# Optimization experiments

Measured on AMD Instinct MI355X. Metric: run time of the kernel, lower is better.

Reference implementation:

```python
import jax, jax.numpy as jnp
import numpy as np

V, B, NT, EN, EMB, ODIM = 5000, 512, 50, 200, 200, 40
PERP = 30.0
BETA_TEMP = 0.2
SINKHORN_ALPHA = 20.0
WEIGHT_ECR = 250.0
ECR_ITERS = 100
SNE_ITERS = 20
EPS_DIV = 1e-16


def _pairwise_sq(x, y):
    # ||x_i||^2 + ||y_j||^2 - 2 x_i . y_j  (matches module's pairwise_euclidean_distance)
    return (jnp.sum(x * x, axis=1)[:, None] + jnp.sum(y * y, axis=1)[None, :]
            - 2.0 * (x @ y.T))


def _bn_train(x, g, b):
    # BatchNorm1d, training mode: batch statistics, biased variance
    m = x.mean(axis=0)
    v = x.var(axis=0)
    return (x - m) / jnp.sqrt(v + 1e-5) * g + b


def _snekhorn_reduce(X, proj):
    # SNEkhorn-style symmetric entropic affinity on rows of X (log-domain
    # symmetric Sinkhorn with uniform marginals), followed by a linear readout
    # to ODIM dims. X: (n, d) -> (n, ODIM).
    C = _pairwise_sq(X, X)                       # (n, n)
    n = X.shape[0]
    eps = jnp.mean(C) / jnp.log(PERP) + 1e-6     # bandwidth tied to perplexity
    log_a = -jnp.log(float(n))                   # uniform target marginal

    @jax.checkpoint
    def step(f, _):
        lse = jax.nn.logsumexp((f[None, :] - C) / eps, axis=1)
        f = 0.5 * (f + eps * (log_a - lse))      # symmetric Sinkhorn update
        return f, None

    f, _ = jax.lax.scan(step, jnp.zeros(n, C.dtype), None, length=SNE_ITERS)
    P = jnp.exp((f[:, None] + f[None, :] - C) / eps)  # (n, n) affinity
    return P @ proj                                   # (n, ODIM)


def _ecr_loss(cost):
    # ECR: entropic OT between topic and word embeddings (fixed-iteration Sinkhorn)
    Km = jnp.exp(-cost * SINKHORN_ALPHA)          # (NT, V)
    a = jnp.full((NT, 1), 1.0 / NT, cost.dtype)
    bm = jnp.full((V, 1), 1.0 / V, cost.dtype)

    def step(u, _):
        v = bm / (Km.T @ u + EPS_DIV)
        u = a / (Km @ v + EPS_DIV)
        return u, None

    u, _ = jax.lax.scan(step, jnp.full((NT, 1), 1.0 / NT, cost.dtype), None,
                        length=ECR_ITERS)
    v = bm / (Km.T @ u + EPS_DIV)
    transp = u * (Km * v.T)
    return WEIGHT_ECR * jnp.sum(transp * cost)


def setup_inputs() -> dict:
    key = jax.random.key(0)
    ks = jax.random.split(key, 12)

    def nrm(k, shape, s=0.02):
        return jax.random.normal(k, shape, jnp.float32) * s

    word_emb = jax.random.normal(ks[0], (V, EMB), jnp.float32)
    word_emb = word_emb / jnp.linalg.norm(word_emb, axis=1, keepdims=True)
    topic_emb = jax.random.normal(ks[1], (NT, EMB), jnp.float32) * 0.1
    topic_emb = topic_emb / jnp.linalg.norm(topic_emb, axis=1, keepdims=True)

    return dict(
        bow=jax.random.uniform(ks[2], (B, V), jnp.float32),
        eps_noise=jax.random.normal(ks[3], (ODIM, NT), jnp.float32),
        W1=nrm(ks[4], (EN, V)), b1=jnp.zeros(EN, jnp.float32),
        W2=nrm(ks[5], (EN, EN)), b2=jnp.zeros(EN, jnp.float32),
        Wmu=nrm(ks[6], (NT, EN)), bmu=jnp.zeros(NT, jnp.float32),
        Wlv=nrm(ks[7], (NT, EN)), blv=jnp.zeros(NT, jnp.float32),
        g_mu=jnp.ones(NT, jnp.float32), be_mu=jnp.zeros(NT, jnp.float32),
        g_lv=jnp.ones(NT, jnp.float32), be_lv=jnp.zeros(NT, jnp.float32),
        g_dec=jnp.ones(V, jnp.float32), be_dec=jnp.zeros(V, jnp.float32),
        word_emb=word_emb, topic_emb=topic_emb,
        proj_V=nrm(ks[8], (V, ODIM), 1.0),
        proj_K=nrm(ks[9], (NT, ODIM), 1.0),
    )


def reference(bow, eps_noise, W1, b1, W2, b2, Wmu, bmu, Wlv, blv,
              g_mu, be_mu, g_lv, be_lv, g_dec, be_dec,
              word_emb, topic_emb, proj_V, proj_K):
    # bow_reduced = SNEkhorn(bow.T).T : (ODIM, V)
    bow_reduced = _snekhorn_reduce(bow.T, proj_V).T

    # encoder1: Linear -> softplus -> Linear -> softplus
    e1 = jax.nn.softplus(bow_reduced @ W1.T + b1)
    e1 = jax.nn.softplus(e1 @ W2.T + b2)
    mu = _bn_train(e1 @ Wmu.T + bmu, g_mu, be_mu)        # (ODIM, NT)
    logvar = _bn_train(e1 @ Wlv.T + blv, g_lv, be_lv)

    z = mu + eps_noise * jnp.exp(0.5 * logvar)           # reparameterize (training)
    theta = jax.nn.softmax(z, axis=1)                    # (ODIM, NT)
    theta_reduced = _snekhorn_reduce(theta.T, proj_K).T  # (ODIM, NT)

    # KL vs logistic-normal prior; with a = ones: mu2 = 0, var2 = 1 - 1/NT
    var2 = 1.0 - 1.0 / NT
    var = jnp.exp(logvar)
    kld = 0.5 * ((var / var2 + mu * mu / var2 + jnp.log(var2) - logvar).sum(axis=1) - NT)
    loss_KL = kld.mean()

    # beta + decode (cost computed once; torch code computes it twice identically)
    cost = _pairwise_sq(topic_emb, word_emb)             # (NT, V)
    beta = jax.nn.softmax(-cost / BETA_TEMP, axis=0)
    recon = jax.nn.softmax(_bn_train(theta_reduced @ beta, g_dec, be_dec), axis=-1)
    recon_loss = -(bow_reduced * jnp.log(recon)).sum(axis=1).mean()

    loss_TM = recon_loss + loss_KL
    loss_ECR = _ecr_loss(cost)
    loss = loss_TM + loss_ECR
    return loss, loss_TM, loss_ECR, theta_reduced
```

## Files before the change

kernel.cpp:

```cpp
#include <hip/hip_runtime.h>
#include <hip/hip_bf16.h>
#include <hip/hip_fp16.h>

#define VV 5000
#define NTOP 50
#define ENH 200
#define NEMB 200
#define OD 40
#define MP 5120
#define KNS 5008

typedef __attribute__((ext_vector_type(8))) short short8;
typedef __attribute__((ext_vector_type(4))) float f32x4;

constexpr size_t OFF_R      = 0;
constexpr size_t OFF_S      = 20224;
constexpr size_t OFF_SCAL   = 22528;
constexpr size_t OFF_PHIA   = 22784;
constexpr size_t OFF_PHIB   = 43008;
constexpr size_t OFF_ROWS   = 63232;
constexpr size_t OFF_PARTS  = 63744;
constexpr size_t OFF_FLAGS  = 71936;
constexpr size_t OFF_MUPRE  = 72960;
constexpr size_t OFF_LVPRE  = 81152;
constexpr size_t OFF_E1T    = 89344;
constexpr size_t OFF_E2T    = 121600;
constexpr size_t OFF_THRED  = 153856;
constexpr size_t OFF_BOWRED = 162048;
constexpr size_t ZERO_BYTES = 962304;
constexpr size_t OFF_PVT    = 962304;
constexpr size_t OFF_XB     = 1453824;
constexpr size_t OFF_CE     = 6696704;
constexpr size_t OFF_COST   = 56696832;
constexpr size_t OFF_KM     = 57697024;
constexpr size_t OFF_BETA   = 58697216;
constexpr size_t OFF_RN     = 59697408;

__device__ __forceinline__ void ecr_block(int b, int it_base, int n_iters, bool do_final,
    const __half* __restrict__ Kn, const float* __restrict__ cost,
    float* __restrict__ acc, int* __restrict__ cnt, float* __restrict__ scal,
    char* smem){
  __half* KmL = (__half*)smem;
  float* varr = (float*)(smem + 32208);
  float* us   = (float*)(smem + 33488);
  float* p5   = (float*)(smem + 33696);
  float* redr = (float*)(smem + 34736);
  const int t = threadIdx.x;
  const int base = (b < 8) ? b*313 : 2504 + (b-8)*312;
  const int sz   = (b < 8) ? 313 : 312;
  for (int c = t; c < 322; c += 256){
    if (c < sz){
      #pragma unroll
      for (int q = 0; q < NTOP; ++q)
        KmL[q*322 + c] = Kn[(size_t)q*KNS + base + c];
    } else {
      #pragma unroll
      for (int q = 0; q < NTOP; ++q) KmL[q*322 + c] = __float2half(0.f);
    }
  }
  if (t < 52){
    float u0 = 0.f;
    if (t < NTOP){
      if (it_base == 0) u0 = 1.f/(float)NTOP;
      else {
        float sm = __hip_atomic_load(&acc[((it_base-1)%3)*64 + t],
                                     __ATOMIC_RELAXED, __HIP_MEMORY_SCOPE_AGENT);
        u0 = (1.f/(float)NTOP)/(sm + 1e-16f);
      }
    }
    us[t] = u0;
  }
  for (int c = sz + t; c < 320; c += 256) varr[c] = 0.f;
  __syncthreads();
  const bool act = (2*t < sz);
  for (int k = 0; k < n_iters; ++k){
    const int g = it_base + k;
    if (act){
      float w0 = 0.f, w1 = 0.f, w2 = 0.f, w3 = 0.f;
      #pragma unroll
      for (int q = 0; q < NTOP; q += 2){
        float u0 = us[q], u1 = us[q+1];
        float2 f0 = __half22float2(*(const __half2*)(KmL + q*322 + 2*t));
        float2 f1 = __half22float2(*(const __half2*)(KmL + (q+1)*322 + 2*t));
        w0 += f0.x*u0; w1 += f0.y*u0;
        w2 += f1.x*u1; w3 += f1.y*u1;
      }
      float2 vv;
      vv.x = (1.f/(float)VV)/((w0+w2) + 1e-16f);
      vv.y = (2*t+1 < sz) ? (1.f/(float)VV)/((w1+w3) + 1e-16f) : 0.f;
      *(float2*)(varr + 2*t) = vv;
    }
    __syncthreads();
    if (t < 250){
      const int qq = t % NTOP, stripe = t / NTOP;
      const __half* kp = KmL + qq*322 + stripe*64;
      const float* vp = varr + stripe*64;
      float s0 = 0.f, s1 = 0.f, s2 = 0.f, s3 = 0.f;
      #pragma unroll
      for (int n = 0; n < 64; n += 4){
        float2 fa = __half22float2(*(const __half2*)(kp + n));
        float2 fb = __half22float2(*(const __half2*)(kp + n + 2));
        float4 v4 = *(const float4*)(vp + n);
        s0 += fa.x*v4.x; s1 += fa.y*v4.y; s2 += fb.x*v4.z; s3 += fb.y*v4.w;
      }
      p5[stripe*52 + qq] = (s0+s1)+(s2+s3);
    }
    __syncthreads();
    if (t < NTOP){
      float sm = p5[t] + p5[52+t] + p5[104+t] + p5[156+t] + p5[208+t];
      __hip_atomic_fetch_add(&acc[(g%3)*64 + t], sm,
                             __ATOMIC_RELAXED, __HIP_MEMORY_SCOPE_AGENT);
    }
    __asm__ volatile("s_waitcnt vmcnt(0)" ::: "memory");
    if (t == 0){
      __hip_atomic_fetch_add(cnt, 1, __ATOMIC_RELEASE, __HIP_MEMORY_SCOPE_AGENT);
      const int tgt = 16*(g+1);
      while (__hip_atomic_load(cnt, __ATOMIC_ACQUIRE, __HIP_MEMORY_SCOPE_AGENT) < tgt)
        __builtin_amdgcn_s_sleep(1);
    }
    if (t < NTOP){
      float sm = __hip_atomic_load(&acc[(g%3)*64 + t],
                                   __ATOMIC_RELAXED, __HIP_MEMORY_SCOPE_AGENT);
      us[t] = (1.f/(float)NTOP)/(sm + 1e-16f);
    }
    if (t < 64)
      __hip_atomic_store(&acc[((g+2)%3)*64 + t], 0.f,
                         __ATOMIC_RELAXED, __HIP_MEMORY_SCOPE_AGENT);
    __syncthreads();
  }
  if (!do_final) return;
  float lsum = 0.f;
  if (act){
    float w0 = 0.f, w1 = 0.f, w2 = 0.f, w3 = 0.f;
    #pragma unroll
    for (int q = 0; q < NTOP; q += 2){
      float u0 = us[q], u1 = us[q+1];
      float2 f0 = __half22float2(*(const __half2*)(KmL + q*322 + 2*t));
      float2 f1 = __half22float2(*(const __half2*)(KmL + (q+1)*322 + 2*t));
      w0 += f0.x*u0; w1 += f0.y*u0;
      w2 += f1.x*u1; w3 += f1.y*u1;
    }
    float v0 = (1.f/(float)VV)/((w0+w2) + 1e-16f);
    const bool ok1 = (2*t+1 < sz);
    float v1 = ok1 ? (1.f/(float)VV)/((w1+w3) + 1e-16f) : 0.f;
    float accv = 0.f;
    #pragma unroll
    for (int q = 0; q < NTOP; ++q){
      float2 f = __half22float2(*(const __half2*)(KmL + q*322 + 2*t));
      float uq = us[q];
      float c0 = cost[(size_t)q*VV + base + 2*t];
      accv += uq*f.x*v0*c0;
      if (ok1){
        float c1 = cost[(size_t)q*VV + base + 2*t + 1];
        accv += uq*f.y*v1*c1;
      }
    }
    lsum = accv;
  }
  #pragma unroll
  for (int off = 32; off; off >>= 1) lsum += __shfl_down(lsum, off, 64);
  if ((t & 63) == 0) redr[t >> 6] = lsum;
  __syncthreads();
  if (t == 0) atomicAdd(&scal[3], redr[0]+redr[1]+redr[2]+redr[3]);
}

__global__ __launch_bounds__(256) void k1_stats(const float* __restrict__ bow,
    __hip_bfloat16* __restrict__ Xb, float* __restrict__ r, float* __restrict__ s,
    const __half* __restrict__ Kn, const float* __restrict__ cost,
    float* __restrict__ accg, int* __restrict__ cnt, float* __restrict__ scal){
  __shared__ __align__(16) char smem[34816];
  const int t = threadIdx.x;
  if (blockIdx.x >= 40){
    int b = (blockIdx.x - 40)*8 + blockIdx.y;
    ecr_block(b, 0, 15, false, Kn, cost, accg, cnt, scal, smem);
    return;
  }
  float (*lds)[129] = (float(*)[129])smem;
  const int i0 = blockIdx.x * 128, d0 = blockIdx.y * 64;
  #pragma unroll
  for (int m = 0; m < 32; ++m){
    int idx = m*256 + t;
    int di = idx >> 7;
    int ii = idx & 127;
    int gi = i0 + ii;
    lds[di][ii] = (gi < VV) ? bow[(size_t)(d0+di)*VV + gi] : 0.f;
  }
  __syncthreads();
  if (t < 128 && (i0 + t) < VV){
    float acc = 0.f;
    for (int di = 0; di < 64; ++di){ float v = lds[di][t]; acc += v*v; }
    atomicAdd(&r[i0+t], acc);
  }
  if (t < 64){
    float acc = 0.f;
    for (int ii = 0; ii < 128; ++ii) acc += lds[t][ii];
    atomicAdd(&s[d0+t], acc);
  }
  __syncthreads();
  #pragma unroll
  for (int m = 0; m < 32; ++m){
    int idx = m*256 + t;
    int ii = idx >> 6;
    int dd = idx & 63;
    Xb[(size_t)(i0+ii)*512 + d0 + dd] = __float2bfloat16(lds[dd][ii]);
  }
}

__global__ __launch_bounds__(256) void k2_eps(const float* __restrict__ r,
    const float* __restrict__ s, float* __restrict__ scal){
  const int t = threadIdx.x;
  float a = 0.f, b = 0.f;
  for (int i = t; i < VV; i += 256) a += r[i];
  for (int d = t; d < 512; d += 256){ float v = s[d]; b += v*v; }
  #pragma unroll
  for (int off = 32; off; off >>= 1){
    a += __shfl_down(a, off, 64);
    b += __shfl_down(b, off, 64);
  }
  __shared__ float ra[4], rb[4];
  int lane = t & 63, w = t >> 6;
  if (lane == 0){ ra[w] = a; rb[w] = b; }
  __syncthreads();
  if (t == 0){
    float sa = ra[0]+ra[1]+ra[2]+ra[3];
    float sb = rb[0]+rb[1]+rb[2]+rb[3];
    float meanC = 2.f*sa/(float)VV - 2.f*sb/((float)VV*(float)VV);
    float eps = meanC / logf(30.f) + 1e-6f;
    scal[0] = eps;
    scal[1] = 1.f/eps;
  }
}

__global__ __launch_bounds__(256) void k3_gemm_ecr(const __hip_bfloat16* __restrict__ Xb,
    const float* __restrict__ r, float* __restrict__ scal, __half* __restrict__ Ce,
    const __half* __restrict__ Kn, const float* __restrict__ cost,
    float* __restrict__ accg, int* __restrict__ cnt){
  __shared__ __align__(16) char smem[36864];
  if (blockIdx.x < 16){
    ecr_block(blockIdx.x, 15, 25, false, Kn, cost, accg, cnt, scal, smem);
    return;
  }
  __hip_bfloat16* As = (__hip_bfloat16*)smem;
  __hip_bfloat16* Bs = (__hip_bfloat16*)(smem + 128*72*2);
  const int b2 = blockIdx.x - 16;
  const int t = threadIdx.x;
  const int i0 = (b2 % 40) * 128, j0 = (b2 / 40) * 128;
  const int lane = t & 63, w = t >> 6;
  const int wr = w >> 1, wc = w & 1;
  const int m16 = lane & 15, q4 = lane >> 4;
  f32x4 acc[4][4];
  #pragma unroll
  for (int a = 0; a < 4; ++a)
    #pragma unroll
    for (int b = 0; b < 4; ++b) acc[a][b] = (f32x4){0.f,0.f,0.f,0.f};
  const int srow = t >> 3, sseg = t & 7;
  for (int kc = 0; kc < 512; kc += 64){
    __syncthreads();
    #pragma unroll
    for (int m = 0; m < 4; ++m){
      int row = m*32 + srow;
      uint4 va = *(const uint4*)(Xb + (size_t)(i0+row)*512 + kc + sseg*8);
      *(uint4*)(As + row*72 + sseg*8) = va;
      uint4 vb = *(const uint4*)(Xb + (size_t)(j0+row)*512 + kc + sseg*8);
      *(uint4*)(Bs + row*72 + sseg*8) = vb;
    }
    __syncthreads();
    #pragma unroll
    for (int ks = 0; ks < 64; ks += 32){
      short8 af[4], bf[4];
      #pragma unroll
      for (int f = 0; f < 4; ++f){
        af[f] = *(const short8*)(As + (wr*64 + f*16 + m16)*72 + ks + q4*8);
        bf[f] = *(const short8*)(Bs + (wc*64 + f*16 + m16)*72 + ks + q4*8);
      }
      #pragma unroll
      for (int fr = 0; fr < 4; ++fr)
        #pragma unroll
        for (int fc = 0; fc < 4; ++fc)
          acc[fr][fc] = __builtin_amdgcn_mfma_f32_16x16x32_bf16(af[fr], bf[fc], acc[fr][fc], 0, 0, 0);
    }
  }
  const float inv_eps = scal[1];
  #pragma unroll
  for (int fr = 0; fr < 4; ++fr){
    int rbase = i0 + wr*64 + fr*16 + q4*4;
    #pragma unroll
    for (int fc = 0; fc < 4; ++fc){
      int col = j0 + wc*64 + fc*16 + m16;
      if (col < VV){
        float rc = r[col];
        #pragma unroll
        for (int q = 0; q < 4; ++q){
          int row = rbase + q;
          if (row < VV){
            float val = (r[row] + rc - 2.f*acc[fr][fc][q]) * inv_eps;
            Ce[(size_t)row*VV + col] = __float2half(val);
          }
        }
      }
    }
  }
}

__global__ __launch_bounds__(256) void k4_sweep_ecr(const __half* __restrict__ Ce,
    const float* __restrict__ phi_prev, float* __restrict__ phi_cur,
    const float* __restrict__ ssum_prev, float* __restrict__ ssum_next,
    float* __restrict__ ssum_zero,
    const __half* __restrict__ Kn, const float* __restrict__ cost,
    float* __restrict__ accg, int* __restrict__ cnt, float* __restrict__ scal,
    int it_base, int g){
  __shared__ __align__(16) char smem[34816];
  const int t = threadIdx.x;
  if (blockIdx.x < 16){
    ecr_block(blockIdx.x, it_base, 2, false, Kn, cost, accg, cnt, scal, smem);
    return;
  }
  const int sb = blockIdx.x - 16;
  const int i0 = (sb >> 1) * 8;
  const int h  = sb & 1;
  const int u0 = h ? 312 : 0;
  const int u1 = h ? 625 : 312;
  const int jbase = u0 * 8;
  const int ncol = (u1 - u0) * 8;
  float* pj  = (float*)smem;
  float* red = (float*)smem + 2504;
  const float loga = -8.517193191416238f;
  for (int j = t; j < ncol; j += 256){
    int gj = jbase + j;
    pj[j] = (g == 0) ? 0.f
          : 0.5f*(phi_prev[gj] + loga - __logf(ssum_prev[gj]));
  }
  if (g > 0 && sb < 20 && t < 250){
    int i = sb*250 + t;
    phi_cur[i] = 0.5f*(phi_prev[i] + loga - __logf(ssum_prev[i]));
  }
  if (sb >= 20 && sb < 40 && t < 250)
    ssum_zero[(sb-20)*250 + t] = 0.f;
  __syncthreads();
  float acc[8];
  #pragma unroll
  for (int rr = 0; rr < 8; ++rr) acc[rr] = 0.f;
  const uint4* ce0 = (const uint4*)(Ce + (size_t)i0*VV);
  for (int u = u0 + t; u < u1; u += 256){
    int lj = (u - u0)*8;
    float p[8];
    #pragma unroll
    for (int e = 0; e < 8; ++e) p[e] = pj[lj + e];
    #pragma unroll
    for (int rr = 0; rr < 8; ++rr){
      uint4 v = ce0[(size_t)rr*625 + u];
      const __half2* hp = (const __half2*)&v;
      float2 c0 = __half22float2(hp[0]);
      float2 c1 = __half22float2(hp[1]);
      float2 c2 = __half22float2(hp[2]);
      float2 c3 = __half22float2(hp[3]);
      acc[rr] += __expf(p[0] - c0.x) + __expf(p[1] - c0.y)
               + __expf(p[2] - c1.x) + __expf(p[3] - c1.y)
               + __expf(p[4] - c2.x) + __expf(p[5] - c2.y)
               + __expf(p[6] - c3.x) + __expf(p[7] - c3.y);
    }
  }
  #pragma unroll
  for (int rr = 0; rr < 8; ++rr)
    #pragma unroll
    for (int off = 32; off; off >>= 1)
      acc[rr] += __shfl_down(acc[rr], off, 64);
  int lane = t & 63, w = t >> 6;
  if (lane == 0){
    #pragma unroll
    for (int rr = 0; rr < 8; ++rr) red[w*8 + rr] = acc[rr];
  }
  __syncthreads();
  if (t < 8){
    float psum = red[t] + red[8+t] + red[16+t] + red[24+t];
    atomicAdd(&ssum_next[i0 + t], psum);
  }
}

__global__ __launch_bounds__(256) void k5p_pvt(const float* __restrict__ projV,
    __hip_bfloat16* __restrict__ pvt, const float* __restrict__ phi19,
    const float* __restrict__ ssum19, float* __restrict__ phiF){
  const int t = threadIdx.x;
  if (blockIdx.x < 20){
    if (t < 250){
      int i = blockIdx.x*250 + t;
      phiF[i] = 0.5f*(phi19[i] + (-8.517193191416238f) - __logf(ssum19[i]));
    }
    return;
  }
  int idx = (blockIdx.x - 20)*256 + t;
  if (idx >= 48*MP) return;
  int n = idx / MP, j = idx - n*MP;
  float v = (n < OD && j < VV) ? projV[(size_t)j*OD + n] : 0.f;
  pvt[idx] = __float2bfloat16(v);
}

__global__ __launch_bounds__(256) void k5_bowred(const __half* __restrict__ Ce,
    const float* __restrict__ phi, const __hip_bfloat16* __restrict__ pvt,
    float* __restrict__ brpA, float* __restrict__ brpC, float* __restrict__ brpD,
    const __half* __restrict__ Kn, const float* __restrict__ cost,
    float* __restrict__ accg, int* __restrict__ cnt, float* __restrict__ scal){
  __shared__ __align__(16) char smem[34816];
  const int t = threadIdx.x;
  if (blockIdx.x >= 40){
    int b = (blockIdx.x - 40)*8 + blockIdx.y;
    ecr_block(b, 80, 15, false, Kn, cost, accg, cnt, scal, smem);
    return;
  }
  __hip_bfloat16* As = (__hip_bfloat16*)smem;
  __hip_bfloat16* Bs = (__hip_bfloat16*)(smem + 18432);
  const int i0 = blockIdx.x * 128;
  const int k0 = blockIdx.y * 640;
  const int lane = t & 63, w = t >> 6;
  const int m16 = lane & 15, q4 = lane >> 4;
  f32x4 acc[2][3];
  #pragma unroll
  for (int a = 0; a < 2; ++a)
    #pragma unroll
    for (int b = 0; b < 3; ++b) acc[a][b] = (f32x4){0.f,0.f,0.f,0.f};
  for (int kc = k0; kc < k0 + 640; kc += 64){
    __syncthreads();
    #pragma unroll
    for (int m = 0; m < 4; ++m){
      int g = m*256 + t;
      int row = g >> 3, cg = g & 7;
      int gi = i0 + row, j2 = kc + cg*8;
      union { __hip_bfloat16 h[8]; short8 v; } u;
      if (gi < VV && j2 < VV){
        uint4 vce = *(const uint4*)(Ce + (size_t)gi*VV + j2);
        const __half2* hp = (const __half2*)&vce;
        float pb = phi[gi];
        float4 pj0 = *(const float4*)(phi + j2);
        float4 pj1 = *(const float4*)(phi + j2 + 4);
        float pj[8] = {pj0.x,pj0.y,pj0.z,pj0.w,pj1.x,pj1.y,pj1.z,pj1.w};
        #pragma unroll
        for (int e = 0; e < 4; ++e){
          float2 ce = __half22float2(hp[e]);
          u.h[2*e]   = __float2bfloat16(__expf(pb + pj[2*e]   - ce.x));
          u.h[2*e+1] = __float2bfloat16(__expf(pb + pj[2*e+1] - ce.y));
        }
      } else {
        #pragma unroll
        for (int e = 0; e < 8; ++e) u.h[e] = __float2bfloat16(0.f);
      }
      *(short8*)(As + row*72 + cg*8) = u.v;
    }
    #pragma unroll
    for (int m = 0; m < 12; ++m){
      int idx = m*256 + t;
      int row = idx >> 6, c = idx & 63;
      Bs[row*72 + c] = pvt[(size_t)row*MP + kc + c];
    }
    __syncthreads();
    #pragma unroll
    for (int ks = 0; ks < 64; ks += 32){
      short8 af[2], bf[3];
      #pragma unroll
      for (int f = 0; f < 2; ++f)
        af[f] = *(const short8*)(As + (w*32 + f*16 + m16)*72 + ks + q4*8);
      #pragma unroll
      for (int f = 0; f < 3; ++f)
        bf[f] = *(const short8*)(Bs + (f*16 + m16)*72 + ks + q4*8);
      #pragma unroll
      for (int fr = 0; fr < 2; ++fr)
        #pragma unroll
        for (int fc = 0; fc < 3; ++fc)
          acc[fr][fc] = __builtin_amdgcn_mfma_f32_16x16x32_bf16(af[fr], bf[fc], acc[fr][fc], 0, 0, 0);
    }
  }
  __syncthreads();
  float* LF = (float*)smem;
  #pragma unroll
  for (int fr = 0; fr < 2; ++fr){
    int lr = w*32 + fr*16 + q4*4;
    #pragma unroll
    for (int fc = 0; fc < 3; ++fc){
      int col = fc*16 + m16;
      #pragma unroll
      for (int q = 0; q < 4; ++q)
        LF[col*133 + lr + q] = acc[fr][fc][q];
    }
  }
  __syncthreads();
  float* brp = (blockIdx.y < 6) ? brpA + (size_t)blockIdx.y*200000
             : (blockIdx.y == 6) ? brpC : brpD;
  for (int o = t; o < OD*128; o += 256){
    int col = o >> 7, row = o & 127;
    int gr = i0 + row;
    if (gr < VV) brp[(size_t)col*VV + gr] = LF[col*133 + row];
  }
}

__global__ __launch_bounds__(256) void k5r_red(const float* __restrict__ brpA,
    const float* __restrict__ brpC, const float* __restrict__ brpD,
    float* __restrict__ br){
  int idx = blockIdx.x*256 + threadIdx.x;
  if (idx >= 50000) return;
  const float4* a = (const float4*)brpA;
  float4 s = a[idx];
  #pragma unroll
  for (int sl = 1; sl < 6; ++sl){
    float4 v = a[(size_t)sl*50000 + idx];
    s.x += v.x; s.y += v.y; s.z += v.z; s.w += v.w;
  }
  {
    float4 v = ((const float4*)brpC)[idx];
    s.x += v.x; s.y += v.y; s.z += v.z; s.w += v.w;
  }
  {
    float4 v = ((const float4*)brpD)[idx];
    s.x += v.x; s.y += v.y; s.z += v.z; s.w += v.w;
  }
  ((float4*)br)[idx] = s;
}

__global__ __launch_bounds__(256) void k6_e1(const float* __restrict__ br,
    const float* __restrict__ W1, float* __restrict__ e1pre,
    const __half* __restrict__ Kn, const float* __restrict__ cost,
    float* __restrict__ accg, int* __restrict__ cnt, float* __restrict__ scal){
  __shared__ __align__(16) char smem[34816];
  const int t = threadIdx.x;
  if (blockIdx.y == 10){
    if (blockIdx.x < 16)
      ecr_block(blockIdx.x, 95, 5, true, Kn, cost, accg, cnt, scal, smem);
    return;
  }
  const int lane = t & 63, w = t >> 6;
  const int k = blockIdx.x*4 + w;
  const int f0 = blockIdx.y * 125;
  float acc[OD];
  #pragma unroll
  for (int i = 0; i < OD; ++i) acc[i] = 0.f;
  const float4* w4p = (const float4*)(W1 + (size_t)k*VV);
  for (int f4 = f0 + lane; f4 < f0 + 125; f4 += 64){
    float4 wv = w4p[f4];
    #pragma unroll
    for (int i = 0; i < OD; ++i){
      float4 bv = ((const float4*)(br + (size_t)i*VV))[f4];
      acc[i] += bv.x*wv.x + bv.y*wv.y + bv.z*wv.z + bv.w*wv.w;
    }
  }
  #pragma unroll
  for (int i = 0; i < OD; ++i)
    #pragma unroll
    for (int off = 32; off; off >>= 1)
      acc[i] += __shfl_down(acc[i], off, 64);
  float (*red)[OD] = (float(*)[OD])smem;
  if (lane == 0){
    #pragma unroll
    for (int i = 0; i < OD; ++i) red[w][i] = acc[i];
  }
  __syncthreads();
  if (t < 160){
    int ww = t / OD, i = t - ww*OD;
    int kk = blockIdx.x*4 + ww;
    atomicAdd(&e1pre[kk*OD + i], red[ww][i]);
  }
}

__global__ __launch_bounds__(256) void k6b_sp(const float* __restrict__ b1,
    float* __restrict__ e1t){
  int idx = blockIdx.x*256 + threadIdx.x;
  if (idx >= ENH*OD) return;
  int kk = idx / OD;
  float x = e1t[idx] + b1[kk];
  e1t[idx] = (x > 20.f) ? x : log1pf(__expf(x));
}

__global__ __launch_bounds__(256) void k7_e2(const float* __restrict__ e1t,
    const float* __restrict__ W2, const float* __restrict__ b2, float* __restrict__ e2t){
  const int t = threadIdx.x;
  const int lane = t & 63, w = t >> 6;
  const int k = blockIdx.x*4 + w;
  float acc[OD];
  #pragma unroll
  for (int i = 0; i < OD; ++i) acc[i] = 0.f;
  for (int j = lane; j < ENH; j += 64){
    float wv = W2[(size_t)k*ENH + j];
    #pragma unroll
    for (int i = 0; i < OD; ++i) acc[i] += e1t[j*OD + i] * wv;
  }
  #pragma unroll
  for (int i = 0; i < OD; ++i)
    #pragma unroll
    for (int off = 32; off; off >>= 1)
      acc[i] += __shfl_down(acc[i], off, 64);
  __shared__ float red[4][OD];
  if (lane == 0){
    #pragma unroll
    for (int i = 0; i < OD; ++i) red[w][i] = acc[i];
  }
  __syncthreads();
  if (t < 160){
    int ww = t / OD, i = t - ww*OD;
    int kk = blockIdx.x*4 + ww;
    float x = red[ww][i] + b2[kk];
    float sp = (x > 20.f) ? x : log1pf(__expf(x));
    e2t[kk*OD + i] = sp;
  }
}

__global__ __launch_bounds__(256) void k8a_mulv(const float* __restrict__ e2t,
    const float* __restrict__ Wmu, const float* __restrict__ bmu,
    const float* __restrict__ Wlv, const float* __restrict__ blv,
    float* __restrict__ mupre, float* __restrict__ lvpre){
  int id = blockIdx.x*256 + threadIdx.x;
  if (id >= NTOP*OD) return;
  int t50 = id / OD, i = id - t50*OD;
  float am = 0.f, al = 0.f;
  for (int kk = 0; kk < ENH; ++kk){
    float e = e2t[kk*OD + i];
    am += e * Wmu[t50*ENH + kk];
    al += e * Wlv[t50*ENH + kk];
  }
  mupre[t50*OD + i] = am + bmu[t50];
  lvpre[t50*OD + i] = al + blv[t50];
}

__global__ __launch_bounds__(256) void k8b_theta(const float* __restrict__ mupre,
    const float* __restrict__ lvpre,
    const float* __restrict__ g_mu, const float* __restrict__ be_mu,
    const float* __restrict__ g_lv, const float* __restrict__ be_lv,
    const float* __restrict__ eps_noise, const float* __restrict__ projK,
    float* __restrict__ thred, float* __restrict__ d_out3, float* __restrict__ scal){
  __shared__ float mu[NTOP][OD];
  __shared__ float lv[NTOP][OD];
  __shared__ float th[OD][NTOP];
  __shared__ float C2[NTOP][NTOP];
  __shared__ float P2[NTOP][NTOP];
  __shared__ float f2[NTOP], nf[NTOP];
  __shared__ float sred[4];
  __shared__ float eps2s[2];
  const int t = threadIdx.x;
  if (t < NTOP){
    float m = 0.f;
    for (int i = 0; i < OD; ++i) m += mupre[t*OD + i];
    m *= (1.f/OD);
    float v = 0.f;
    for (int i = 0; i < OD; ++i){ float d = mupre[t*OD+i] - m; v += d*d; }
    v *= (1.f/OD);
    float sc = g_mu[t] * rsqrtf(v + 1e-5f);
    float sh = be_mu[t];
    for (int i = 0; i < OD; ++i) mu[t][i] = (mupre[t*OD+i] - m)*sc + sh;
    m = 0.f;
    for (int i = 0; i < OD; ++i) m += lvpre[t*OD + i];
    m *= (1.f/OD);
    v = 0.f;
    for (int i = 0; i < OD; ++i){ float d = lvpre[t*OD+i] - m; v += d*d; }
    v *= (1.f/OD);
    sc = g_lv[t] * rsqrtf(v + 1e-5f);
    sh = be_lv[t];
    for (int i = 0; i < OD; ++i) lv[t][i] = (lvpre[t*OD+i] - m)*sc + sh;
  }
  __syncthreads();
  {
    float kl = 0.f;
    if (t < OD){
      const float var2 = 1.f - 1.f/(float)NTOP;
      const float lv2 = logf(var2);
      float ssum = 0.f;
      for (int q = 0; q < NTOP; ++q){
        float l = lv[q][t];
        float m = mu[q][t];
        ssum += (__expf(l) + m*m)/var2 + lv2 - l;
      }
      kl = 0.5f*(ssum - (float)NTOP);
    }
    #pragma unroll
    for (int off = 32; off; off >>= 1) kl += __shfl_down(kl, off, 64);
    if ((t & 63) == 0) sred[t >> 6] = kl;
    __syncthreads();
    if (t == 0) scal[2] = (sred[0]+sred[1]+sred[2]+sred[3]) * (1.f/OD);
    __syncthreads();
  }
  if (t < OD){
    float z[NTOP];
    float mx = -1e30f;
    for (int q = 0; q < NTOP; ++q){
      float val = mu[q][t] + eps_noise[t*NTOP + q]*__expf(0.5f*lv[q][t]);
      z[q] = val;
      mx = fmaxf(mx, val);
    }
    float ssum = 0.f;
    for (int q = 0; q < NTOP; ++q){ float e = __expf(z[q]-mx); z[q] = e; ssum += e; }
    float inv = 1.f/ssum;
    for (int q = 0; q < NTOP; ++q) th[t][q] = z[q]*inv;
  }
  __syncthreads();
  {
    float csum = 0.f;
    for (int pr = t; pr < NTOP*NTOP; pr += 256){
      int a = pr / NTOP, b = pr - (pr/NTOP)*NTOP;
      float ss = 0.f;
      for (int i = 0; i < OD; ++i){ float d = th[i][a] - th[i][b]; ss += d*d; }
      C2[a][b] = ss;
      csum += ss;
    }
    #pragma unroll
    for (int off = 32; off; off >>= 1) csum += __shfl_down(csum, off, 64);
    if ((t & 63) == 0) sred[t >> 6] = csum;
    __syncthreads();
    if (t == 0){
      float meanC = (sred[0]+sred[1]+sred[2]+sred[3]) / ((float)NTOP*NTOP);
      float e2 = meanC / logf(30.f) + 1e-6f;
      eps2s[0] = e2; eps2s[1] = 1.f/e2;
    }
  }
  if (t < NTOP) f2[t] = 0.f;
  __syncthreads();
  const float loga2 = -logf((float)NTOP);
  for (int it = 0; it < 20; ++it){
    if (t < NTOP){
      float ie = eps2s[1];
      float ssum = 0.f;
      for (int sI = 0; sI < NTOP; ++sI)
        ssum += __expf((f2[sI] - C2[t][sI]) * ie);
      float lse = __logf(ssum);
      nf[t] = 0.5f*(f2[t] + eps2s[0]*(loga2 - lse));
    }
    __syncthreads();
    if (t < NTOP) f2[t] = nf[t];
    __syncthreads();
  }
  for (int pr = t; pr < NTOP*NTOP; pr += 256){
    int a = pr / NTOP, b = pr - (pr/NTOP)*NTOP;
    P2[a][b] = __expf((f2[a] + f2[b] - C2[a][b]) * eps2s[1]);
  }
  __syncthreads();
  for (int o = t; o < NTOP*OD; o += 256){
    int t50 = o / OD, kk = o - (o/OD)*OD;
    float ssum = 0.f;
    for (int sI = 0; sI < NTOP; ++sI)
      ssum += P2[t50][sI] * projK[sI*OD + kk];
    thred[kk*NTOP + t50] = ssum;
    d_out3[kk*NTOP + t50] = ssum;
  }
}

__global__ __launch_bounds__(256) void k10_cost(const float* __restrict__ temb,
    const float* __restrict__ wemb, float* __restrict__ cost, __half* __restrict__ Kn,
    float* __restrict__ beta){
  __shared__ float Tt[100][52];
  __shared__ float wed[100][68];
  __shared__ float sc[52][64];
  __shared__ float tn[52];
  __shared__ float wn[64];
  const int t = threadIdx.x;
  const int j0 = blockIdx.x * 64;
  const int tg = t >> 4, jg = t & 15;
  float am[4][4];
  #pragma unroll
  for (int a = 0; a < 4; ++a)
    #pragma unroll
    for (int b = 0; b < 4; ++b) am[a][b] = 0.f;
  float tnp = 0.f, wnp = 0.f;
  for (int c = 0; c < 2; ++c){
    __syncthreads();
    const int dbase = c*100;
    for (int idx = t; idx < NTOP*100; idx += 256){
      int t50 = idx / 100, d = idx - t50*100;
      Tt[d][t50] = temb[t50*NEMB + dbase + d];
    }
    for (int idx = t; idx < 64*100; idx += 256){
      int j = idx / 100, d = idx - j*100;
      int gj = j0 + j;
      wed[d][j] = (gj < VV) ? wemb[(size_t)gj*NEMB + dbase + d] : 0.f;
    }
    __syncthreads();
    if (t < NTOP){
      float a = 0.f;
      for (int d = 0; d < 100; ++d){ float v = Tt[d][t]; a += v*v; }
      tnp += a;
    }
    if (t >= 64 && t < 128){
      int j = t - 64;
      float a = 0.f;
      for (int d = 0; d < 100; ++d){ float v = wed[d][j]; a += v*v; }
      wnp += a;
    }
    if (t < 208){
      for (int d = 0; d < 100; ++d){
        const float4 tv = *(const float4*)(&Tt[d][tg*4]);
        const float4 wv = *(const float4*)(&wed[d][jg*4]);
        am[0][0] += tv.x*wv.x; am[0][1] += tv.x*wv.y; am[0][2] += tv.x*wv.z; am[0][3] += tv.x*wv.w;
        am[1][0] += tv.y*wv.x; am[1][1] += tv.y*wv.y; am[1][2] += tv.y*wv.z; am[1][3] += tv.y*wv.w;
        am[2][0] += tv.z*wv.x; am[2][1] += tv.z*wv.y; am[2][2] += tv.z*wv.z; am[2][3] += tv.z*wv.w;
        am[3][0] += tv.w*wv.x; am[3][1] += tv.w*wv.y; am[3][2] += tv.w*wv.z; am[3][3] += tv.w*wv.w;
      }
    }
  }
  if (t < NTOP) tn[t] = tnp;
  if (t >= 64 && t < 128) wn[t-64] = wnp;
  __syncthreads();
  if (t < 208){
    #pragma unroll
    for (int a = 0; a < 4; ++a){
      int t50 = tg*4 + a;
      if (t50 < NTOP){
        float tv = tn[t50];
        float cc[4];
        #pragma unroll
        for (int b = 0; b < 4; ++b) cc[b] = tv + wn[jg*4+b] - 2.f*am[a][b];
        int gj = j0 + jg*4;
        if (gj + 3 < VV)
          *(float4*)(cost + (size_t)t50*VV + gj) = make_float4(cc[0],cc[1],cc[2],cc[3]);
        #pragma unroll
        for (int b = 0; b < 4; ++b) sc[t50][jg*4+b] = -5.f*cc[b];
      }
    }
  }
  __syncthreads();
  if (t < 64){
    int gj = j0 + t;
    if (gj < VV){
      float mx = -1e30f;
      for (int q = 0; q < NTOP; ++q) mx = fmaxf(mx, sc[q][t]);
      float ssum = 0.f;
      for (int q = 0; q < NTOP; ++q){ float e = __expf(sc[q][t]-mx); sc[q][t] = e; ssum += e; }
      float inv = 1.f/ssum;
      for (int q = 0; q < NTOP; ++q){
        float e = sc[q][t];
        float e2 = e*e;
        Kn[(size_t)q*KNS + gj] = __float2half(e2*e2);
        beta[(size_t)q*VV + gj] = e*inv;
      }
    }
  }
}

__global__ __launch_bounds__(256) void k12_reconA(const float* __restrict__ thred,
    const float* __restrict__ beta, const float* __restrict__ g_dec,
    const float* __restrict__ be_dec, float* __restrict__ Rn){
  __shared__ float trs[OD][NTOP];
  const int t = threadIdx.x;
  for (int o = t; o < OD*NTOP; o += 256) trs[o/NTOP][o - (o/NTOP)*NTOP] = thred[o];
  __syncthreads();
  int j = blockIdx.x*256 + t;
  if (j >= VV) return;
  float a[OD];
  #pragma unroll
  for (int i = 0; i < OD; ++i) a[i] = 0.f;
  for (int q = 0; q < NTOP; ++q){
    float bv = beta[(size_t)q*VV + j];
    #pragma unroll
    for (int i = 0; i < OD; ++i) a[i] += trs[i][q]*bv;
  }
  float m = 0.f;
  #pragma unroll
  for (int i = 0; i < OD; ++i) m += a[i];
  m *= (1.f/OD);
  float v = 0.f;
  #pragma unroll
  for (int i = 0; i < OD; ++i){ float d = a[i]-m; v += d*d; }
  v *= (1.f/OD);
  float scale = g_dec[j]*rsqrtf(v + 1e-5f);
  float sh = be_dec[j];
  #pragma unroll
  for (int i = 0; i < OD; ++i) Rn[(size_t)i*VV + j] = (a[i]-m)*scale + sh;
}

__global__ __launch_bounds__(256) void k13_reconB(const float* __restrict__ Rn,
    const float* __restrict__ br, float* __restrict__ rows){
  const int i = blockIdx.x;
  const int t = threadIdx.x;
  float s1 = 0.f, s2 = 0.f, s3 = 0.f;
  for (int j = t; j < VV; j += 256){
    float rn = Rn[(size_t)i*VV + j];
    float bv = br[(size_t)i*VV + j];
    s1 += __expf(rn);
    s2 += bv*rn;
    s3 += bv;
  }
  #pragma unroll
  for (int off = 32; off; off >>= 1){
    s1 += __shfl_down(s1, off, 64);
    s2 += __shfl_down(s2, off, 64);
    s3 += __shfl_down(s3, off, 64);
  }
  __shared__ float red[3][4];
  int lane = t & 63, w = t >> 6;
  if (lane == 0){ red[0][w] = s1; red[1][w] = s2; red[2][w] = s3; }
  __syncthreads();
  if (t == 0){
    rows[i]      = red[0][0]+red[0][1]+red[0][2]+red[0][3];
    rows[40 + i] = red[1][0]+red[1][1]+red[1][2]+red[1][3];
    rows[80 + i] = red[2][0]+red[2][1]+red[2][2]+red[2][3];
  }
}

__global__ void k14_final(const float* __restrict__ rows, const float* __restrict__ scal,
    float* __restrict__ out){
  const int t = threadIdx.x;
  float v = 0.f;
  if (t < OD) v = rows[40 + t] - logf(rows[t]) * rows[80 + t];
  #pragma unroll
  for (int off = 32; off; off >>= 1) v += __shfl_down(v, off, 64);
  if (t == 0){
    float recon = -v * (1.f/OD);
    float tm = recon + scal[2];
    float ecr = 250.f * scal[3];
    out[0] = tm + ecr;
    out[1] = tm;
    out[2] = ecr;
  }
}

extern "C" void kernel_launch(void* const* d_in, const int* in_sizes, int n_in,
                              void* d_out, int out_size, void* d_ws, size_t ws_size,
                              hipStream_t stream){
  const float* bow   = (const float*)d_in[0];
  const float* epsn  = (const float*)d_in[1];
  const float* W1    = (const float*)d_in[2];
  const float* b1    = (const float*)d_in[3];
  const float* W2    = (const float*)d_in[4];
  const float* b2    = (const float*)d_in[5];
  const float* Wmu   = (const float*)d_in[6];
  const float* bmu   = (const float*)d_in[7];
  const float* Wlv   = (const float*)d_in[8];
  const float* blv   = (const float*)d_in[9];
  const float* g_mu  = (const float*)d_in[10];
  const float* be_mu = (const float*)d_in[11];
  const float* g_lv  = (const float*)d_in[12];
  const float* be_lv = (const float*)d_in[13];
  const float* g_dec = (const float*)d_in[14];
  const float* be_dec= (const float*)d_in[15];
  const float* wemb  = (const float*)d_in[16];
  const float* temb  = (const float*)d_in[17];
  const float* projV = (const float*)d_in[18];
  const float* projK = (const float*)d_in[19];
  char* ws = (char*)d_ws;
  float* r     = (float*)(ws + OFF_R);
  float* s     = (float*)(ws + OFF_S);
  float* scal  = (float*)(ws + OFF_SCAL);
  float* phiA  = (float*)(ws + OFF_PHIA);
  float* phiB  = (float*)(ws + OFF_PHIB);
  float* rows  = (float*)(ws + OFF_ROWS);
  float* accg  = (float*)(ws + OFF_PARTS);
  int*   cnt   = (int*)(ws + OFF_FLAGS);
  float* mupre = (float*)(ws + OFF_MUPRE);
  float* lvpre = (float*)(ws + OFF_LVPRE);
  float* e1t   = (float*)(ws + OFF_E1T);
  float* e2t   = (float*)(ws + OFF_E2T);
  float* thred = (float*)(ws + OFF_THRED);
  float* br    = (float*)(ws + OFF_BOWRED);
  __hip_bfloat16* pvt = (__hip_bfloat16*)(ws + OFF_PVT);
  __hip_bfloat16* Xb  = (__hip_bfloat16*)(ws + OFF_XB);
  __half* Ce   = (__half*)(ws + OFF_CE);
  float* cost  = (float*)(ws + OFF_COST);
  __half* Kn   = (__half*)(ws + OFF_KM);
  float* beta  = (float*)(ws + OFF_BETA);
  float* Rn    = (float*)(ws + OFF_RN);
  float* sbuf0 = (float*)(ws + OFF_RN);
  float* sbuf1 = (float*)(ws + OFF_RN + 20224);
  float* sbuf2 = (float*)(ws + OFF_RN + 40448);
  float* sbuf[3] = {sbuf0, sbuf1, sbuf2};
  float* P2b[2] = {phiA, phiB};
  float* brpA  = (float*)(ws + OFF_XB);
  float* brpC  = (float*)(ws + OFF_RN);
  float* brpD  = (float*)(ws + OFF_BOWRED);
  float* out   = (float*)d_out;

  hipMemsetAsync(d_ws, 0, ZERO_BYTES, stream);
  hipMemsetAsync(ws + OFF_RN, 0, 60672, stream);
  k10_cost<<<79, 256, 0, stream>>>(temb, wemb, cost, Kn, beta);
  k1_stats<<<dim3(42, 8), 256, 0, stream>>>(bow, Xb, r, s, Kn, cost, accg, cnt, scal);
  k2_eps<<<1, 256, 0, stream>>>(r, s, scal);
  k3_gemm_ecr<<<1616, 256, 0, stream>>>(Xb, r, scal, Ce, Kn, cost, accg, cnt);
  for (int g = 0; g < 20; ++g){
    k4_sweep_ecr<<<1266, 256, 0, stream>>>(Ce,
        P2b[(g+1)&1] , P2b[g&1] ,
        sbuf[g%3], sbuf[(g+1)%3], sbuf[(g+2)%3],
        Kn, cost, accg, cnt, scal, 40 + 2*g, g);
  }
  k5p_pvt<<<980, 256, 0, stream>>>(projV, pvt, phiB, sbuf[2], phiA);
  k5_bowred<<<dim3(42, 8), 256, 0, stream>>>(Ce, phiA, pvt, brpA, brpC, brpD,
                                             Kn, cost, accg, cnt, scal);
  k5r_red<<<196, 256, 0, stream>>>(brpA, brpC, brpD, br);
  k6_e1<<<dim3(50, 11), 256, 0, stream>>>(br, W1, e1t, Kn, cost, accg, cnt, scal);
  k6b_sp<<<32, 256, 0, stream>>>(b1, e1t);
  k7_e2<<<50, 256, 0, stream>>>(e1t, W2, b2, e2t);
  k8a_mulv<<<8, 256, 0, stream>>>(e2t, Wmu, bmu, Wlv, blv, mupre, lvpre);
  k8b_theta<<<1, 256, 0, stream>>>(mupre, lvpre, g_mu, be_mu, g_lv, be_lv,
                                   epsn, projK, thred, out + 3, scal);
  k12_reconA<<<20, 256, 0, stream>>>(thred, beta, g_dec, be_dec, Rn);
  k13_reconB<<<40, 256, 0, stream>>>(Rn, br, rows);
  k14_final<<<1, 64, 0, stream>>>(rows, scal, out);
}
```

Before: 887.8 us.

## Exploit symmetry of the SNE cost matrix in Sinkhorn sweeps

The per-iteration Sinkhorn logsumexp sweep now tiles the 5000x5000 half-precision cost matrix into 128x128 blocks and visits only the upper triangle (820 tiles). Each off-diagonal tile adds to both its row sums and its column sums, which should roughly halve the reads of the cost matrix per iteration. In exchange, off-diagonal tiles do twice the exponentials, and extra LDS transposes and atomics are added. The ECR iteration split across kernels is rebalanced to match the shorter sweep kernels.

```diff
diff --git a/kernel.cpp b/kernel.cpp
--- a/kernel.cpp
+++ b/kernel.cpp
@@ -172,7 +172,7 @@
   const int t = threadIdx.x;
   if (blockIdx.x >= 40){
     int b = (blockIdx.x - 40)*8 + blockIdx.y;
-    ecr_block(b, 0, 15, false, Kn, cost, accg, cnt, scal, smem);
+    ecr_block(b, 0, 10, false, Kn, cost, accg, cnt, scal, smem);
     return;
   }
   float (*lds)[129] = (float(*)[129])smem;
@@ -237,7 +237,7 @@
     float* __restrict__ accg, int* __restrict__ cnt){
   __shared__ __align__(16) char smem[36864];
   if (blockIdx.x < 16){
-    ecr_block(blockIdx.x, 15, 25, false, Kn, cost, accg, cnt, scal, smem);
+    ecr_block(blockIdx.x, 10, 25, false, Kn, cost, accg, cnt, scal, smem);
     return;
   }
   __hip_bfloat16* As = (__hip_bfloat16*)smem;
@@ -302,7 +302,7 @@
   }
 }
 
-__global__ __launch_bounds__(256) void k4_sweep_ecr(const __half* __restrict__ Ce,
+__global__ __launch_bounds__(256) void k4_symsweep(const __half* __restrict__ Ce,
     const float* __restrict__ phi_prev, float* __restrict__ phi_cur,
     const float* __restrict__ ssum_prev, float* __restrict__ ssum_next,
     float* __restrict__ ssum_zero,
@@ -315,65 +315,84 @@
     ecr_block(blockIdx.x, it_base, 2, false, Kn, cost, accg, cnt, scal, smem);
     return;
   }
-  const int sb = blockIdx.x - 16;
-  const int i0 = (sb >> 1) * 8;
-  const int h  = sb & 1;
-  const int u0 = h ? 312 : 0;
-  const int u1 = h ? 625 : 312;
-  const int jbase = u0 * 8;
-  const int ncol = (u1 - u0) * 8;
-  float* pj  = (float*)smem;
-  float* red = (float*)smem + 2504;
   const float loga = -8.517193191416238f;
-  for (int j = t; j < ncol; j += 256){
-    int gj = jbase + j;
-    pj[j] = (g == 0) ? 0.f
-          : 0.5f*(phi_prev[gj] + loga - __logf(ssum_prev[gj]));
-  }
-  if (g > 0 && sb < 20 && t < 250){
-    int i = sb*250 + t;
-    phi_cur[i] = 0.5f*(phi_prev[i] + loga - __logf(ssum_prev[i]));
-  }
-  if (sb >= 20 && sb < 40 && t < 250)
-    ssum_zero[(sb-20)*250 + t] = 0.f;
-  __syncthreads();
-  float acc[8];
-  #pragma unroll
-  for (int rr = 0; rr < 8; ++rr) acc[rr] = 0.f;
-  const uint4* ce0 = (const uint4*)(Ce + (size_t)i0*VV);
-  for (int u = u0 + t; u < u1; u += 256){
-    int lj = (u - u0)*8;
-    float p[8];
-    #pragma unroll
-    for (int e = 0; e < 8; ++e) p[e] = pj[lj + e];
-    #pragma unroll
-    for (int rr = 0; rr < 8; ++rr){
-      uint4 v = ce0[(size_t)rr*625 + u];
+  int bt = blockIdx.x - 16;
+  int bi = 0, rem = bt;
+  while (rem >= 40 - bi){ rem -= 40 - bi; ++bi; }
+  const int bj = bi + rem;
+  const bool diag = (bi == bj);
+  const int i0 = bi*128, j0 = bj*128;
+  float* phiI = (float*)smem;
+  float* phiJ = (float*)smem + 128;
+  float* RL   = (float*)smem + 256;
+  if (t < 128){
+    int gi = i0 + t;
+    float ph = 0.f;
+    if (gi < VV && g > 0)
+      ph = 0.5f*(phi_prev[gi] + loga - __logf(ssum_prev[gi]));
+    phiI[t] = ph;
+    if (diag && gi < VV){
+      phi_cur[gi] = ph;
+      ssum_zero[gi] = 0.f;
+    }
+  } else {
+    int gj = j0 + (t - 128);
+    float ph = 0.f;
+    if (gj < VV && g > 0)
+      ph = 0.5f*(phi_prev[gj] + loga - __logf(ssum_prev[gj]));
+    phiJ[t-128] = ph;
+  }
+  __syncthreads();
+  const int rg = t >> 4, cg = t & 15;
+  const int jb = j0 + cg*8;
+  const bool colok = jb < VV;
+  float pj[8];
+  #pragma unroll
+  for (int e = 0; e < 8; ++e) pj[e] = phiJ[cg*8 + e];
+  float rowacc[8], colacc[8];
+  #pragma unroll
+  for (int x = 0; x < 8; ++x){ rowacc[x] = 0.f; colacc[x] = 0.f; }
+  #pragma unroll
+  for (int rr = 0; rr < 8; ++rr){
+    int rloc = rg*8 + rr;
+    int gi = i0 + rloc;
+    if (gi < VV && colok){
+      uint4 v = *(const uint4*)(Ce + (size_t)gi*VV + jb);
       const __half2* hp = (const __half2*)&v;
-      float2 c0 = __half22float2(hp[0]);
-      float2 c1 = __half22float2(hp[1]);
-      float2 c2 = __half22float2(hp[2]);
-      float2 c3 = __half22float2(hp[3]);
-      acc[rr] += __expf(p[0] - c0.x) + __expf(p[1] - c0.y)
-               + __expf(p[2] - c1.x) + __expf(p[3] - c1.y)
-               + __expf(p[4] - c2.x) + __expf(p[5] - c2.y)
-               + __expf(p[6] - c3.x) + __expf(p[7] - c3.y);
-    }
-  }
-  #pragma unroll
-  for (int rr = 0; rr < 8; ++rr)
-    #pragma unroll
-    for (int off = 32; off; off >>= 1)
-      acc[rr] += __shfl_down(acc[rr], off, 64);
-  int lane = t & 63, w = t >> 6;
-  if (lane == 0){
-    #pragma unroll
-    for (int rr = 0; rr < 8; ++rr) red[w*8 + rr] = acc[rr];
-  }
-  __syncthreads();
-  if (t < 8){
-    float psum = red[t] + red[8+t] + red[16+t] + red[24+t];
-    atomicAdd(&ssum_next[i0 + t], psum);
+      float pI = phiI[rloc];
+      #pragma unroll
+      for (int e = 0; e < 4; ++e){
+        float2 c = __half22float2(hp[e]);
+        rowacc[rr] += __expf(pj[2*e] - c.x) + __expf(pj[2*e+1] - c.y);
+        if (!diag){
+          colacc[2*e]   += __expf(pI - c.x);
+          colacc[2*e+1] += __expf(pI - c.y);
+        }
+      }
+    }
+  }
+  #pragma unroll
+  for (int rr = 0; rr < 8; ++rr) RL[(rg*8+rr)*17 + cg] = rowacc[rr];
+  __syncthreads();
+  if (t < 128){
+    float sm = 0.f;
+    #pragma unroll
+    for (int c2 = 0; c2 < 16; ++c2) sm += RL[t*17 + c2];
+    int gi = i0 + t;
+    if (gi < VV) atomicAdd(&ssum_next[gi], sm);
+  }
+  if (!diag){
+    __syncthreads();
+    #pragma unroll
+    for (int cc = 0; cc < 8; ++cc) RL[(cg*8+cc)*17 + rg] = colacc[cc];
+    __syncthreads();
+    if (t < 128){
+      float sm = 0.f;
+      #pragma unroll
+      for (int r2 = 0; r2 < 16; ++r2) sm += RL[t*17 + r2];
+      int gj = j0 + t;
+      if (gj < VV) atomicAdd(&ssum_next[gj], sm);
+    }
   }
 }
 
@@ -404,7 +423,7 @@
   const int t = threadIdx.x;
   if (blockIdx.x >= 40){
     int b = (blockIdx.x - 40)*8 + blockIdx.y;
-    ecr_block(b, 80, 15, false, Kn, cost, accg, cnt, scal, smem);
+    ecr_block(b, 75, 20, false, Kn, cost, accg, cnt, scal, smem);
     return;
   }
   __hip_bfloat16* As = (__hip_bfloat16*)smem;
@@ -967,10 +986,10 @@
   k2_eps<<<1, 256, 0, stream>>>(r, s, scal);
   k3_gemm_ecr<<<1616, 256, 0, stream>>>(Xb, r, scal, Ce, Kn, cost, accg, cnt);
   for (int g = 0; g < 20; ++g){
-    k4_sweep_ecr<<<1266, 256, 0, stream>>>(Ce,
+    k4_symsweep<<<836, 256, 0, stream>>>(Ce,
         P2b[(g+1)&1] , P2b[g&1] ,
         sbuf[g%3], sbuf[(g+1)%3], sbuf[(g+2)%3],
-        Kn, cost, accg, cnt, scal, 40 + 2*g, g);
+        Kn, cost, accg, cnt, scal, 35 + 2*g, g);
   }
   k5p_pvt<<<980, 256, 0, stream>>>(projV, pvt, phiB, sbuf[2], phiA);
   k5_bowred<<<dim3(42, 8), 256, 0, stream>>>(Ce, phiA, pvt, brpA, brpC, brpD,
```

Result: faster. 770.0 us (-13.3%).
